# Optimization experiments

Hardware: AMD Instinct MI355X
Metric: run time of the kernel (lower is better)

Reference implementation:

```python
import jax, jax.numpy as jnp
from jax import lax
import numpy as np

D_COND = 48      # d_condition
K = 24           # n_bins
HID = 128        # hidden_dim
T = 10           # n_transforms
TAIL = 15.0      # tail_bound
B = 131072       # batch (contexts x samples flattened, as in sample())


def setup_inputs() -> dict:
    key = jax.random.key(0)
    ks = jax.random.split(key, 8)
    def w(k, shape, fan_in, gain=1.0):
        return (jax.random.normal(k, shape, jnp.float32) * (gain / np.sqrt(fan_in))).astype(jnp.float32)
    return {
        "z": jax.random.normal(ks[0], (B,), jnp.float32),
        "context": jax.random.normal(ks[1], (B, D_COND), jnp.float32),
        "W0": w(ks[2], (T, D_COND, HID), D_COND),
        "b0": jnp.zeros((T, HID), jnp.float32),
        "W1": w(ks[3], (T, HID, HID), HID),
        "b1": jnp.zeros((T, HID), jnp.float32),
        "W2": w(ks[4], (T, HID, HID), HID),
        "b2": jnp.zeros((T, HID), jnp.float32),
        "W3": w(ks[5], (T, HID, 3 * K + 1), HID, gain=0.1),
        "b3": jnp.zeros((T, 3 * K + 1), jnp.float32),
        "loc": jnp.float32(85.0),
        "scale": jnp.float32(5.0),
    }


def _spline_forward(x, widths, heights, derivs):
    # x: (B,); widths/heights: (B,K); derivs: (B,K+1)
    inside = (x >= -TAIL) & (x <= TAIL)
    cw = jnp.pad(jnp.cumsum(widths, -1), ((0, 0), (1, 0)), constant_values=-TAIL)   # (B,K+1)
    ch = jnp.pad(jnp.cumsum(heights, -1), ((0, 0), (1, 0)), constant_values=-TAIL)  # (B,K+1)
    # torch.searchsorted(cw[...,1:], x, right=False) == count of elems < x
    idx = jnp.clip(jnp.sum(cw[:, 1:] < x[:, None], axis=-1), 0, K - 1)
    take = lambda a, i: jnp.take_along_axis(a, i[:, None], axis=-1)[:, 0]
    w_k = take(widths, idx)
    h_k = take(heights, idx)
    cw_k = take(cw, idx)
    ch_k = take(ch, idx)
    d_k = take(derivs, idx)
    d_k1 = take(derivs, idx + 1)
    s = h_k / w_k
    xi = jnp.clip((x - cw_k) / w_k, 1e-6, 1.0 - 1e-6)
    one_m = 1.0 - xi
    numer = h_k * (s * xi * xi + d_k * xi * one_m)
    denom = s + (d_k + d_k1 - 2.0 * s) * xi * one_m
    y = ch_k + numer / denom
    dy_dxi = s * s * (d_k1 * xi * xi + 2.0 * s * xi * one_m + d_k * one_m * one_m) / (denom * denom)
    log_det = (jnp.log(jnp.maximum(dy_dxi, 1e-10))
               + jnp.log(jnp.maximum(h_k, 1e-10))
               - jnp.log(jnp.maximum(w_k, 1e-10)))
    y = jnp.where(inside, y, x)
    log_det = jnp.where(inside, log_det, 0.0)
    return y, log_det


def reference(z, context, W0, b0, W1, b1, W2, b2, W3, b3, loc, scale):
    def body(carry, p):
        zc, ld = carry
        w0, c0, w1, c1, w2, c2, w3, c3 = p
        h = jax.nn.silu(context @ w0 + c0)
        h = jax.nn.silu(h @ w1 + c1)
        h = jax.nn.silu(h @ w2 + c2)
        params = h @ w3 + c3                                   # (B, 3K+1)
        Wl, Hl, Dl = params[:, :K], params[:, K:2 * K], params[:, 2 * K:]
        widths = jax.nn.softmax(Wl, axis=-1) * (2.0 * TAIL)
        heights = jax.nn.softmax(Hl, axis=-1) * (2.0 * TAIL)
        derivs = jax.nn.softplus(Dl) + 1e-3
        y, l = _spline_forward(zc, widths, heights, derivs)
        return (y, ld + l), None

    (z_out, total_ld), _ = lax.scan(body, (z, jnp.zeros_like(z)),
                                    (W0, b0, W1, b1, W2, b2, W3, b3))
    s = jnp.maximum(scale, 0.1)
    temp_f = z_out * s + loc   # _unstandardize, as in sample()
    return temp_f, total_ld
```

## Files before the change

### kernel.cpp

```cpp
#include <hip/hip_runtime.h>
#include <hip/hip_bf16.h>

#define DCOND 48
#define KBINS 24
#define HID 128
#define TSTEPS 10
#define NPAR 73
#define TAILF 15.0f

typedef __attribute__((ext_vector_type(8))) short v8s;
typedef __attribute__((ext_vector_type(4))) float f32x4;
typedef __attribute__((ext_vector_type(4))) unsigned u32x4;

__device__ __forceinline__ short f2bf(float f) {
    __hip_bfloat16 h = __float2bfloat16(f);
    return __builtin_bit_cast(short, h);
}
__device__ __forceinline__ float bf2f(short s) {
    unsigned u = ((unsigned)(unsigned short)s) << 16;
    return __builtin_bit_cast(float, u);
}
__device__ __forceinline__ float silu_f(float v) {
    return __fdividef(v, 1.0f + __expf(-v));
}

__device__ __forceinline__ unsigned cvt_pk(float a, float b) {
    unsigned r;
    asm("v_cvt_pk_bf16_f32 %0, %1, %2" : "=v"(r) : "v"(a), "v"(b));
    return r;
}

__device__ __forceinline__ void split8(f32x4 a0, f32x4 a1, v8s& hi, v8s& lo) {
    unsigned h0 = cvt_pk(a0[0], a0[1]);
    unsigned h1 = cvt_pk(a0[2], a0[3]);
    unsigned h2 = cvt_pk(a1[0], a1[1]);
    unsigned h3 = cvt_pk(a1[2], a1[3]);
    float l0 = a0[0] - __builtin_bit_cast(float, h0 << 16);
    float l1 = a0[1] - __builtin_bit_cast(float, h0 & 0xffff0000u);
    float l2 = a0[2] - __builtin_bit_cast(float, h1 << 16);
    float l3 = a0[3] - __builtin_bit_cast(float, h1 & 0xffff0000u);
    float l4 = a1[0] - __builtin_bit_cast(float, h2 << 16);
    float l5 = a1[1] - __builtin_bit_cast(float, h2 & 0xffff0000u);
    float l6 = a1[2] - __builtin_bit_cast(float, h3 << 16);
    float l7 = a1[3] - __builtin_bit_cast(float, h3 & 0xffff0000u);
    unsigned q0 = cvt_pk(l0, l1);
    unsigned q1 = cvt_pk(l2, l3);
    unsigned q2 = cvt_pk(l4, l5);
    unsigned q3 = cvt_pk(l6, l7);
    hi = __builtin_bit_cast(v8s, (u32x4){h0, h1, h2, h3});
    lo = __builtin_bit_cast(v8s, (u32x4){q0, q1, q2, q3});
}

__global__ void prep_w(const float* __restrict__ W0, const float* __restrict__ W1,
                       const float* __restrict__ W2, const float* __restrict__ W3,
                       short* __restrict__ ws)
{
    int g = blockIdx.x * 256 + threadIdx.x;
    if (g >= TSTEPS * 51200) return;
    int t = g / 51200;
    int r = g % 51200;

    int base_e, elems, NT, Kreal, Nreal;
    const float* W;
    if (r < 8192)       { base_e = 0;     elems = 8192;  NT = 8; Kreal = 48;  Nreal = 128; W = W0 + (size_t)t * DCOND * HID; }
    else if (r < 24576) { base_e = 8192;  elems = 16384; NT = 8; Kreal = 128; Nreal = 128; W = W1 + (size_t)t * HID * HID; }
    else if (r < 40960) { base_e = 24576; elems = 16384; NT = 8; Kreal = 128; Nreal = 128; W = W2 + (size_t)t * HID * HID; }
    else                { base_e = 40960; elems = 10240; NT = 5; Kreal = 128; Nreal = 73;  W = W3 + (size_t)t * HID * NPAR; }

    int e  = r - base_e;
    int j  = e & 7;
    int ln = (e >> 3) & 63;
    int q  = e >> 9;
    int nt = q % NT, kc = q / NT;
    int k  = kc * 32 + (ln >> 4) * 8 + j;
    int n  = nt * 16 + (ln & 15);

    float v = 0.0f;
    if (k < Kreal && n < Nreal) v = W[(size_t)k * Nreal + n];
    short hi = f2bf(v);
    short lo = f2bf(v - bf2f(hi));

    size_t o = (size_t)t * 102400 + 2 * (size_t)base_e + e;
    ws[o]         = hi;
    ws[o + elems] = lo;
}

#define MBLK 128
#define NTHR 512

template<int ROUNDS>
__device__ __forceinline__ void w_issue(const short* __restrict__ g, int tid, v8s (&r)[8]) {
    #pragma unroll
    for (int i = 0; i < ROUNDS; ++i)
        r[i] = *(const v8s*)(g + tid * 8 + i * 4096);
}
template<int ROUNDS>
__device__ __forceinline__ void w_flush(short* __restrict__ lds, int tid, const v8s (&r)[8]) {
    #pragma unroll
    for (int i = 0; i < ROUNDS; ++i)
        *(v8s*)(lds + tid * 8 + i * 4096) = r[i];
}

template<int KC, int NTN, int NTOT, int ELEMS, bool ACT, bool AREG>
__device__ __forceinline__ void layer_run(const float* __restrict__ bias, int nreal,
                                          char* __restrict__ hb,
                                          const short* __restrict__ Wbh,
                                          int lane, int nb0,
                                          const v8s* cxh, const v8s* cxl)
{
    const int kg = (lane >> 4) * 8;

    v8s ah[2][KC], al[2][KC];
    #pragma unroll
    for (int mt = 0; mt < 2; ++mt) {
        const int arow = mt * 16 + (lane & 15);
        const int asw  = (arow & 7) << 4;
        #pragma unroll
        for (int kc = 0; kc < KC; ++kc) {
            if (AREG) {
                ah[mt][kc] = cxh[mt * KC + kc];
                al[mt][kc] = cxl[mt * KC + kc];
            } else {
                const int kb = (kc * 32 + kg) * 4;
                f32x4 a0 = *(const f32x4*)(hb + arow * 512 + (kb ^ asw));
                f32x4 a1 = *(const f32x4*)(hb + arow * 512 + ((kb + 16) ^ asw));
                split8(a0, a1, ah[mt][kc], al[mt][kc]);
            }
        }
    }

    const int ncol  = lane & 15;
    const int crow  = (lane >> 4) * 4;
    const short* bbase = Wbh + lane * 8;

    #pragma unroll
    for (int np = 0; np < NTN / 2; ++np) {
        const int n0 = nb0 + np * 32 + ncol;
        const int n1 = n0 + 16;
        const float bv0 = (n0 < nreal) ? bias[n0] : 0.0f;
        const float bv1 = (n1 < nreal) ? bias[n1] : 0.0f;
        f32x4 a00 = {bv0, bv0, bv0, bv0}, a01 = {bv1, bv1, bv1, bv1};
        f32x4 a10 = {bv0, bv0, bv0, bv0}, a11 = {bv1, bv1, bv1, bv1};
        #pragma unroll
        for (int kc = 0; kc < KC; ++kc) {
            const short* bp0 = bbase + (kc * NTOT + np * 2) * 512;
            const short* bp1 = bp0 + 512;
            v8s bh0 = *(const v8s*)bp0;
            v8s bl0 = *(const v8s*)(bp0 + ELEMS);
            v8s bh1 = *(const v8s*)bp1;
            v8s bl1 = *(const v8s*)(bp1 + ELEMS);
            a00 = __builtin_amdgcn_mfma_f32_16x16x32_bf16(ah[0][kc], bh0, a00, 0, 0, 0);
            a01 = __builtin_amdgcn_mfma_f32_16x16x32_bf16(ah[0][kc], bh1, a01, 0, 0, 0);
            a10 = __builtin_amdgcn_mfma_f32_16x16x32_bf16(ah[1][kc], bh0, a10, 0, 0, 0);
            a11 = __builtin_amdgcn_mfma_f32_16x16x32_bf16(ah[1][kc], bh1, a11, 0, 0, 0);
            a00 = __builtin_amdgcn_mfma_f32_16x16x32_bf16(ah[0][kc], bl0, a00, 0, 0, 0);
            a01 = __builtin_amdgcn_mfma_f32_16x16x32_bf16(ah[0][kc], bl1, a01, 0, 0, 0);
            a10 = __builtin_amdgcn_mfma_f32_16x16x32_bf16(ah[1][kc], bl0, a10, 0, 0, 0);
            a11 = __builtin_amdgcn_mfma_f32_16x16x32_bf16(ah[1][kc], bl1, a11, 0, 0, 0);
            a00 = __builtin_amdgcn_mfma_f32_16x16x32_bf16(al[0][kc], bh0, a00, 0, 0, 0);
            a01 = __builtin_amdgcn_mfma_f32_16x16x32_bf16(al[0][kc], bh1, a01, 0, 0, 0);
            a10 = __builtin_amdgcn_mfma_f32_16x16x32_bf16(al[1][kc], bh0, a10, 0, 0, 0);
            a11 = __builtin_amdgcn_mfma_f32_16x16x32_bf16(al[1][kc], bh1, a11, 0, 0, 0);
        }
        #pragma unroll
        for (int mt = 0; mt < 2; ++mt) {
            const f32x4 c0 = mt ? a10 : a00;
            const f32x4 c1 = mt ? a11 : a01;
            #pragma unroll
            for (int r = 0; r < 4; ++r) {
                const int row = mt * 16 + crow + r;
                const int sw  = (row & 7) << 4;
                float v0 = c0[r], v1 = c1[r];
                if (ACT) { v0 = silu_f(v0); v1 = silu_f(v1); }
                *(float*)(hb + row * 512 + ((n0 * 4) ^ sw)) = v0;
                *(float*)(hb + row * 512 + ((n1 * 4) ^ sw)) = v1;
            }
        }
    }
    if (NTN & 1) {
        const int n0 = nb0 + (NTN - 1) * 16 + ncol;
        const float bv0 = (n0 < nreal) ? bias[n0] : 0.0f;
        f32x4 a00 = {bv0, bv0, bv0, bv0};
        f32x4 a10 = {bv0, bv0, bv0, bv0};
        #pragma unroll
        for (int kc = 0; kc < KC; ++kc) {
            const short* bp0 = bbase + (kc * NTOT + NTN - 1) * 512;
            v8s bh0 = *(const v8s*)bp0;
            v8s bl0 = *(const v8s*)(bp0 + ELEMS);
            a00 = __builtin_amdgcn_mfma_f32_16x16x32_bf16(ah[0][kc], bh0, a00, 0, 0, 0);
            a10 = __builtin_amdgcn_mfma_f32_16x16x32_bf16(ah[1][kc], bh0, a10, 0, 0, 0);
            a00 = __builtin_amdgcn_mfma_f32_16x16x32_bf16(ah[0][kc], bl0, a00, 0, 0, 0);
            a10 = __builtin_amdgcn_mfma_f32_16x16x32_bf16(ah[1][kc], bl0, a10, 0, 0, 0);
            a00 = __builtin_amdgcn_mfma_f32_16x16x32_bf16(al[0][kc], bh0, a00, 0, 0, 0);
            a10 = __builtin_amdgcn_mfma_f32_16x16x32_bf16(al[1][kc], bh0, a10, 0, 0, 0);
        }
        #pragma unroll
        for (int mt = 0; mt < 2; ++mt) {
            const f32x4 c0 = mt ? a10 : a00;
            #pragma unroll
            for (int r = 0; r < 4; ++r) {
                const int row = mt * 16 + crow + r;
                const int sw  = (row & 7) << 4;
                float v0 = c0[r];
                if (ACT) v0 = silu_f(v0);
                *(float*)(hb + row * 512 + ((n0 * 4) ^ sw)) = v0;
            }
        }
    }
}

__global__ __launch_bounds__(NTHR, 2)
void nsf_mfma(const float* __restrict__ z_g, const float* __restrict__ ctx_g,
              const float* __restrict__ b0g, const float* __restrict__ b1g,
              const float* __restrict__ b2g, const float* __restrict__ b3g,
              const float* __restrict__ locp, const float* __restrict__ sclp,
              const short* __restrict__ wsW, float* __restrict__ out, int B)
{
    __shared__ float Hlds[MBLK * 128];
    __shared__ short Wlds[32768];
    const int tid  = threadIdx.x;
    const int lane = tid & 63, wave = tid >> 6;
    const int p    = wave >> 1, h = wave & 1;
    const int blk  = blockIdx.x;
    char* hb = (char*)Hlds + p * 32 * 512;

    v8s wreg[8];
    w_issue<4>(wsW, tid, wreg);

    v8s cxh[4], cxl[4];
    {
        const int k0 = (lane >> 4) * 8;
        #pragma unroll
        for (int mt = 0; mt < 2; ++mt) {
            int gidr = blk * MBLK + p * 32 + mt * 16 + (lane & 15);
            if (gidr > B - 1) gidr = B - 1;
            const float* cg = ctx_g + (size_t)gidr * DCOND;
            f32x4 c0 = *(const f32x4*)(cg + k0);
            f32x4 c1 = *(const f32x4*)(cg + k0 + 4);
            split8(c0, c1, cxh[mt * 2 + 0], cxl[mt * 2 + 0]);
            if ((lane >> 4) < 2) {
                f32x4 c2 = *(const f32x4*)(cg + 32 + k0);
                f32x4 c3 = *(const f32x4*)(cg + 36 + k0);
                split8(c2, c3, cxh[mt * 2 + 1], cxl[mt * 2 + 1]);
            } else {
                #pragma unroll
                for (int u = 0; u < 8; ++u) { cxh[mt * 2 + 1][u] = 0; cxl[mt * 2 + 1][u] = 0; }
            }
        }
    }

    float x = 0.0f, ld = 0.0f;
    if (lane < 16) {
        int gid = blk * MBLK + p * 32 + h * 16 + lane;
        if (gid > B - 1) gid = B - 1;
        x = z_g[gid];
    }

    #pragma unroll 1
    for (int t = 0; t < TSTEPS; ++t) {
        const short* wstep = wsW + (size_t)t * 102400;
        const short* wnext = wsW + (size_t)((t + 1) % TSTEPS) * 102400;

        w_flush<4>(Wlds, tid, wreg);
        w_issue<8>(wstep + 16384, tid, wreg);
        __syncthreads();

        layer_run<2, 4, 8, 8192, true, true>(b0g + t * HID, HID, hb,
                                             Wlds + h * 2048, lane, h * 64, cxh, cxl);
        __syncthreads();

        w_flush<8>(Wlds, tid, wreg);
        w_issue<8>(wstep + 49152, tid, wreg);
        __syncthreads();

        layer_run<4, 4, 8, 16384, true, false>(b1g + t * HID, HID, hb,
                                               Wlds + h * 2048, lane, h * 64, nullptr, nullptr);
        __syncthreads();

        w_flush<8>(Wlds, tid, wreg);
        w_issue<5>(wstep + 81920, tid, wreg);
        __syncthreads();

        layer_run<4, 4, 8, 16384, true, false>(b2g + t * HID, HID, hb,
                                               Wlds + h * 2048, lane, h * 64, nullptr, nullptr);
        __syncthreads();

        w_flush<5>(Wlds, tid, wreg);
        w_issue<4>(wnext, tid, wreg);
        __syncthreads();

        if (h == 0)
            layer_run<4, 3, 5, 10240, false, false>(b3g + t * NPAR, NPAR, hb,
                                                    Wlds, lane, 0, nullptr, nullptr);
        else
            layer_run<4, 2, 5, 10240, false, false>(b3g + t * NPAR, NPAR, hb,
                                                    Wlds + 1536, lane, 48, nullptr, nullptr);
        __syncthreads();

        if (lane < 16) {
            const int srow = h * 16 + lane;
            const char* hrow = hb + srow * 512;
            const int sw = (srow & 7) << 4;

            float pw[KBINS], ph[KBINS];
            #pragma unroll
            for (int g = 0; g < 6; ++g) {
                f32x4 vw = *(const f32x4*)(hrow + ((g * 16) ^ sw));
                f32x4 vh = *(const f32x4*)(hrow + (((g + 6) * 16) ^ sw));
                #pragma unroll
                for (int u = 0; u < 4; ++u) { pw[g * 4 + u] = vw[u]; ph[g * 4 + u] = vh[u]; }
            }
            float mw = pw[0], mh = ph[0];
            #pragma unroll
            for (int i = 1; i < KBINS; ++i) { mw = fmaxf(mw, pw[i]); mh = fmaxf(mh, ph[i]); }
            float wsum = 0.0f, hsum = 0.0f;
            #pragma unroll
            for (int i = 0; i < KBINS; ++i) {
                pw[i] = __expf(pw[i] - mw); wsum += pw[i];
                ph[i] = __expf(ph[i] - mh); hsum += ph[i];
            }
            const float wmul = __fdividef(2.0f * TAILF, wsum);
            const float hmul = __fdividef(2.0f * TAILF, hsum);

            float cw = 0.0f, ch = 0.0f;
            float cwk = -TAILF, chk = -TAILF;
            float wk = pw[0] * wmul, hk = ph[0] * hmul;
            int idx = 0;
            #pragma unroll
            for (int i = 1; i < KBINS; ++i) {
                cw += pw[i - 1] * wmul;
                ch += ph[i - 1] * hmul;
                if (cw < x) {
                    cwk = cw; chk = ch;
                    wk = pw[i] * wmul; hk = ph[i] * hmul;
                    idx = i;
                }
            }
            float d0 = *(const float*)(hrow + (((2 * KBINS + idx) * 4) ^ sw));
            float d1 = *(const float*)(hrow + (((2 * KBINS + idx + 1) * 4) ^ sw));
            const float dk  = fmaxf(d0, 0.0f) + __logf(1.0f + __expf(-fabsf(d0))) + 0.001f;
            const float dk1 = fmaxf(d1, 0.0f) + __logf(1.0f + __expf(-fabsf(d1))) + 0.001f;

            const bool inside = (x >= -TAILF) && (x <= TAILF);
            const float sr = __fdividef(hk, wk);
            float xi = __fdividef(x - cwk, wk);
            xi = fminf(fmaxf(xi, 1e-6f), 1.0f - 1e-6f);
            const float om  = 1.0f - xi;
            const float xio = xi * om;
            const float numer = hk * (sr * xi * xi + dk * xio);
            const float denom = sr + (dk + dk1 - 2.0f * sr) * xio;
            const float y = chk + __fdividef(numer, denom);
            const float dyd = __fdividef(sr * sr * (dk1 * xi * xi + 2.0f * sr * xio + dk * om * om),
                                         denom * denom);
            const float lg = __logf(fmaxf(dyd, 1e-10f)) + __logf(fmaxf(hk, 1e-10f))
                           - __logf(fmaxf(wk, 1e-10f));
            x  = inside ? y : x;
            ld += inside ? lg : 0.0f;
        }
    }

    if (lane < 16) {
        const int gid = blk * MBLK + p * 32 + h * 16 + lane;
        if (gid < B) {
            const float s = fmaxf(sclp[0], 0.1f);
            out[gid]     = fmaf(x, s, locp[0]);
            out[B + gid] = ld;
        }
    }
}

#define FBLK 256
template<int KIN, int WS, int NOUT, bool ACT>
__device__ __forceinline__ void dense_chunk(const float* __restrict__ W,
                                            const float* __restrict__ bias,
                                            int j0, const float (&hin)[KIN],
                                            float* __restrict__ sb, int tid)
{
    #pragma unroll 1
    for (int jj = 0; jj < NOUT; jj += 8) {
        const int j = j0 + jj;
        float a[8];
        #pragma unroll
        for (int u = 0; u < 8; ++u) a[u] = bias[j + u];
        #pragma unroll
        for (int k = 0; k < KIN; ++k) {
            const float* w = W + k * WS + j;
            const float hk = hin[k];
            #pragma unroll
            for (int u = 0; u < 8; ++u) a[u] = fmaf(hk, w[u], a[u]);
        }
        #pragma unroll
        for (int u = 0; u < 8; ++u) {
            float v = ACT ? silu_f(a[u]) : a[u];
            sb[(jj + u) * FBLK + tid] = v;
        }
    }
}

__global__ __launch_bounds__(FBLK, 2)
void nsf_fwd_slow(const float* __restrict__ z_g, const float* __restrict__ ctx_g,
                  const float* __restrict__ W0g, const float* __restrict__ b0g,
                  const float* __restrict__ W1g, const float* __restrict__ b1g,
                  const float* __restrict__ W2g, const float* __restrict__ b2g,
                  const float* __restrict__ W3g, const float* __restrict__ b3g,
                  const float* __restrict__ locp, const float* __restrict__ sclp,
                  float* __restrict__ out, int B)
{
    __shared__ float sbuf[64 * FBLK];
    const int tid = threadIdx.x;
    const int gid = blockIdx.x * FBLK + tid;
    if (gid >= B) return;
    float x = z_g[gid], ld = 0.0f;
    #pragma unroll 1
    for (int t = 0; t < TSTEPS; ++t) {
        asm volatile("" ::: "memory");
        const float* W0 = W0g + (size_t)t * DCOND * HID;
        const float* b0 = b0g + (size_t)t * HID;
        const float* W1 = W1g + (size_t)t * HID * HID;
        const float* b1 = b1g + (size_t)t * HID;
        const float* W2 = W2g + (size_t)t * HID * HID;
        const float* b2 = b2g + (size_t)t * HID;
        const float* W3 = W3g + (size_t)t * HID * NPAR;
        const float* b3 = b3g + (size_t)t * NPAR;
        float ctx[DCOND];
        #pragma unroll
        for (int k = 0; k < DCOND; ++k) ctx[k] = ctx_g[(size_t)gid * DCOND + k];
        float h[HID];
        dense_chunk<DCOND, HID, 64, true>(W0, b0, 0, ctx, sbuf, tid);
        #pragma unroll
        for (int j = 0; j < 64; ++j) h[j] = sbuf[j * FBLK + tid];
        dense_chunk<DCOND, HID, 64, true>(W0, b0, 64, ctx, sbuf, tid);
        #pragma unroll
        for (int j = 0; j < 64; ++j) h[64 + j] = sbuf[j * FBLK + tid];
        #pragma unroll 1
        for (int l = 0; l < 2; ++l) {
            const float* W  = (l == 0) ? W1 : W2;
            const float* bb = (l == 0) ? b1 : b2;
            float hlo[64];
            dense_chunk<HID, HID, 64, true>(W, bb, 0, h, sbuf, tid);
            #pragma unroll
            for (int j = 0; j < 64; ++j) hlo[j] = sbuf[j * FBLK + tid];
            dense_chunk<HID, HID, 64, true>(W, bb, 64, h, sbuf, tid);
            #pragma unroll
            for (int j = 0; j < 64; ++j) h[64 + j] = sbuf[j * FBLK + tid];
            #pragma unroll
            for (int j = 0; j < 64; ++j) h[j] = hlo[j];
        }
        float p[NPAR];
        dense_chunk<HID, NPAR, 64, false>(W3, b3, 0, h, sbuf, tid);
        #pragma unroll
        for (int j = 0; j < 64; ++j) p[j] = sbuf[j * FBLK + tid];
        dense_chunk<HID, NPAR, 8, false>(W3, b3, 64, h, sbuf, tid);
        #pragma unroll
        for (int j = 0; j < 8; ++j) p[64 + j] = sbuf[j * FBLK + tid];
        {
            float a = b3[72];
            #pragma unroll
            for (int k = 0; k < HID; ++k) a = fmaf(h[k], W3[k * NPAR + 72], a);
            p[72] = a;
        }
        float mw = p[0];
        #pragma unroll
        for (int i = 1; i < KBINS; ++i) mw = fmaxf(mw, p[i]);
        float we[KBINS]; float wsum = 0.0f;
        #pragma unroll
        for (int i = 0; i < KBINS; ++i) { we[i] = __expf(p[i] - mw); wsum += we[i]; }
        const float wmul = __fdividef(2.0f * TAILF, wsum);
        float mh = p[KBINS];
        #pragma unroll
        for (int i = 1; i < KBINS; ++i) mh = fmaxf(mh, p[KBINS + i]);
        float he[KBINS]; float hsum = 0.0f;
        #pragma unroll
        for (int i = 0; i < KBINS; ++i) { he[i] = __expf(p[KBINS + i] - mh); hsum += he[i]; }
        const float hmul = __fdividef(2.0f * TAILF, hsum);
        float dvv[KBINS + 1];
        #pragma unroll
        for (int i = 0; i <= KBINS; ++i) {
            float xd = p[2 * KBINS + i];
            dvv[i] = fmaxf(xd, 0.0f) + __logf(1.0f + __expf(-fabsf(xd))) + 0.001f;
        }
        float cw = 0.0f, ch = 0.0f, cwk = -TAILF, chk = -TAILF;
        float wk = we[0] * wmul, hk = he[0] * hmul, dk = dvv[0], dk1 = dvv[1];
        #pragma unroll
        for (int i = 1; i < KBINS; ++i) {
            cw += we[i - 1] * wmul;
            ch += he[i - 1] * hmul;
            if (cw < x) {
                cwk = cw; chk = ch;
                wk = we[i] * wmul; hk = he[i] * hmul;
                dk = dvv[i]; dk1 = dvv[i + 1];
            }
        }
        const bool inside = (x >= -TAILF) && (x <= TAILF);
        const float sr = __fdividef(hk, wk);
        float xi = __fdividef(x - cwk, wk);
        xi = fminf(fmaxf(xi, 1e-6f), 1.0f - 1e-6f);
        const float om  = 1.0f - xi;
        const float xio = xi * om;
        const float numer = hk * (sr * xi * xi + dk * xio);
        const float denom = sr + (dk + dk1 - 2.0f * sr) * xio;
        const float y = chk + __fdividef(numer, denom);
        const float dyd = __fdividef(sr * sr * (dk1 * xi * xi + 2.0f * sr * xio + dk * om * om),
                                     denom * denom);
        const float lg = __logf(fmaxf(dyd, 1e-10f)) + __logf(fmaxf(hk, 1e-10f))
                       - __logf(fmaxf(wk, 1e-10f));
        x  = inside ? y : x;
        ld += inside ? lg : 0.0f;
    }
    const float s = fmaxf(sclp[0], 0.1f);
    out[gid]     = fmaf(x, s, locp[0]);
    out[B + gid] = ld;
}

extern "C" void kernel_launch(void* const* d_in, const int* in_sizes, int n_in,
                              void* d_out, int out_size, void* d_ws, size_t ws_size,
                              hipStream_t stream) {
    const float* z    = (const float*)d_in[0];
    const float* ctx  = (const float*)d_in[1];
    const float* W0   = (const float*)d_in[2];
    const float* b0   = (const float*)d_in[3];
    const float* W1   = (const float*)d_in[4];
    const float* b1   = (const float*)d_in[5];
    const float* W2   = (const float*)d_in[6];
    const float* b2   = (const float*)d_in[7];
    const float* W3   = (const float*)d_in[8];
    const float* b3   = (const float*)d_in[9];
    const float* loc  = (const float*)d_in[10];
    const float* scl  = (const float*)d_in[11];
    float* out = (float*)d_out;
    const int B = in_sizes[0];

    const size_t ws_need = (size_t)TSTEPS * 102400 * sizeof(short);
    if (ws_size < ws_need) {
        const int nblk = (B + FBLK - 1) / FBLK;
        hipLaunchKernelGGL(nsf_fwd_slow, dim3(nblk), dim3(FBLK), 0, stream,
                           z, ctx, W0, b0, W1, b1, W2, b2, W3, b3, loc, scl, out, B);
        return;
    }

    short* ws = (short*)d_ws;
    const int prep_total = TSTEPS * 51200;
    hipLaunchKernelGGL(prep_w, dim3((prep_total + 255) / 256), dim3(256), 0, stream,
                       W0, W1, W2, W3, ws);

    const int nblk = (B + MBLK - 1) / MBLK;
    hipLaunchKernelGGL(nsf_mfma, dim3(nblk), dim3(NTHR), 0, stream,
                       z, ctx, b0, b1, b2, b3, loc, scl, ws, out, B);
}
```

Baseline: 761.1 us.

## Stage weight panels with direct global-to-LDS loads instead of register prefetch

Replaces the register-held weight prefetch (global load into VGPRs, then flush to LDS) with global_load_lds direct transfers issued after each layer's barrier. The A-operand split is hoisted out of the MFMA routine so it runs while the panel load is in flight. This removes the register staging and the LDS write instructions, which may lower VGPR pressure. The cost is that each weight panel load is now exposed on the critical path between layers instead of being prefetched a full layer ahead, plus an extra barrier per step.

Measured after the change: 651.8 us. -14.4%, faster.

```diff
diff --git a/kernel.cpp b/kernel.cpp
--- a/kernel.cpp
+++ b/kernel.cpp
@@ -88,47 +88,47 @@
 #define MBLK 128
 #define NTHR 512
 
-template<int ROUNDS>
-__device__ __forceinline__ void w_issue(const short* __restrict__ g, int tid, v8s (&r)[8]) {
+template<int NISSUE>
+__device__ __forceinline__ void stage_panel(const short* __restrict__ g,
+                                            short* lds, int tid)
+{
+    const int wuni = (tid >> 6) << 9;
+    const int lofs = tid * 8;
     #pragma unroll
-    for (int i = 0; i < ROUNDS; ++i)
-        r[i] = *(const v8s*)(g + tid * 8 + i * 4096);
-}
-template<int ROUNDS>
-__device__ __forceinline__ void w_flush(short* __restrict__ lds, int tid, const v8s (&r)[8]) {
-    #pragma unroll
-    for (int i = 0; i < ROUNDS; ++i)
-        *(v8s*)(lds + tid * 8 + i * 4096) = r[i];
-}
-
-template<int KC, int NTN, int NTOT, int ELEMS, bool ACT, bool AREG>
-__device__ __forceinline__ void layer_run(const float* __restrict__ bias, int nreal,
-                                          char* __restrict__ hb,
-                                          const short* __restrict__ Wbh,
-                                          int lane, int nb0,
-                                          const v8s* cxh, const v8s* cxl)
+    for (int i = 0; i < NISSUE; ++i) {
+        __builtin_amdgcn_global_load_lds(
+            (const __attribute__((address_space(1))) void*)(g + i * 4096 + lofs),
+            (__attribute__((address_space(3))) void*)(lds + i * 4096 + wuni),
+            16, 0, 0);
+    }
+}
+
+template<int KC>
+__device__ __forceinline__ void a_split(const char* __restrict__ hb, int lane,
+                                        v8s (&ah)[2][4], v8s (&al)[2][4])
 {
     const int kg = (lane >> 4) * 8;
-
-    v8s ah[2][KC], al[2][KC];
     #pragma unroll
     for (int mt = 0; mt < 2; ++mt) {
         const int arow = mt * 16 + (lane & 15);
         const int asw  = (arow & 7) << 4;
         #pragma unroll
         for (int kc = 0; kc < KC; ++kc) {
-            if (AREG) {
-                ah[mt][kc] = cxh[mt * KC + kc];
-                al[mt][kc] = cxl[mt * KC + kc];
-            } else {
-                const int kb = (kc * 32 + kg) * 4;
-                f32x4 a0 = *(const f32x4*)(hb + arow * 512 + (kb ^ asw));
-                f32x4 a1 = *(const f32x4*)(hb + arow * 512 + ((kb + 16) ^ asw));
-                split8(a0, a1, ah[mt][kc], al[mt][kc]);
-            }
-        }
-    }
-
+            const int kb = (kc * 32 + kg) * 4;
+            f32x4 a0 = *(const f32x4*)(hb + arow * 512 + (kb ^ asw));
+            f32x4 a1 = *(const f32x4*)(hb + arow * 512 + ((kb + 16) ^ asw));
+            split8(a0, a1, ah[mt][kc], al[mt][kc]);
+        }
+    }
+}
+
+template<int KC, int NTN, int NTOT, int ELEMS, bool ACT, int AKC>
+__device__ __forceinline__ void layer_mfma(const float* __restrict__ bias, int nreal,
+                                           char* __restrict__ hb,
+                                           const short* __restrict__ Wbh,
+                                           int lane, int nb0,
+                                           const v8s (&ah)[2][AKC], const v8s (&al)[2][AKC])
+{
     const int ncol  = lane & 15;
     const int crow  = (lane >> 4) * 4;
     const short* bbase = Wbh + lane * 8;
@@ -224,10 +224,9 @@
     const int blk  = blockIdx.x;
     char* hb = (char*)Hlds + p * 32 * 512;
 
-    v8s wreg[8];
-    w_issue<4>(wsW, tid, wreg);
-
-    v8s cxh[4], cxl[4];
+    stage_panel<4>(wsW, Wlds, tid);
+
+    v8s cxh[2][2], cxl[2][2];
     {
         const int k0 = (lane >> 4) * 8;
         #pragma unroll
@@ -237,14 +236,14 @@
             const float* cg = ctx_g + (size_t)gidr * DCOND;
             f32x4 c0 = *(const f32x4*)(cg + k0);
             f32x4 c1 = *(const f32x4*)(cg + k0 + 4);
-            split8(c0, c1, cxh[mt * 2 + 0], cxl[mt * 2 + 0]);
+            split8(c0, c1, cxh[mt][0], cxl[mt][0]);
             if ((lane >> 4) < 2) {
                 f32x4 c2 = *(const f32x4*)(cg + 32 + k0);
                 f32x4 c3 = *(const f32x4*)(cg + 36 + k0);
-                split8(c2, c3, cxh[mt * 2 + 1], cxl[mt * 2 + 1]);
+                split8(c2, c3, cxh[mt][1], cxl[mt][1]);
             } else {
                 #pragma unroll
-                for (int u = 0; u < 8; ++u) { cxh[mt * 2 + 1][u] = 0; cxl[mt * 2 + 1][u] = 0; }
+                for (int u = 0; u < 8; ++u) { cxh[mt][1][u] = 0; cxl[mt][1][u] = 0; }
             }
         }
     }
@@ -256,46 +255,48 @@
         x = z_g[gid];
     }
 
+    v8s axh[2][4], axl[2][4];
+
+    __syncthreads();
+
     #pragma unroll 1
     for (int t = 0; t < TSTEPS; ++t) {
         const short* wstep = wsW + (size_t)t * 102400;
         const short* wnext = wsW + (size_t)((t + 1) % TSTEPS) * 102400;
 
-        w_flush<4>(Wlds, tid, wreg);
-        w_issue<8>(wstep + 16384, tid, wreg);
-        __syncthreads();
-
-        layer_run<2, 4, 8, 8192, true, true>(b0g + t * HID, HID, hb,
-                                             Wlds + h * 2048, lane, h * 64, cxh, cxl);
-        __syncthreads();
-
-        w_flush<8>(Wlds, tid, wreg);
-        w_issue<8>(wstep + 49152, tid, wreg);
-        __syncthreads();
-
-        layer_run<4, 4, 8, 16384, true, false>(b1g + t * HID, HID, hb,
-                                               Wlds + h * 2048, lane, h * 64, nullptr, nullptr);
-        __syncthreads();
-
-        w_flush<8>(Wlds, tid, wreg);
-        w_issue<5>(wstep + 81920, tid, wreg);
-        __syncthreads();
-
-        layer_run<4, 4, 8, 16384, true, false>(b2g + t * HID, HID, hb,
-                                               Wlds + h * 2048, lane, h * 64, nullptr, nullptr);
-        __syncthreads();
-
-        w_flush<5>(Wlds, tid, wreg);
-        w_issue<4>(wnext, tid, wreg);
+        layer_mfma<2, 4, 8, 8192, true, 2>(b0g + t * HID, HID, hb,
+                                           Wlds + h * 2048, lane, h * 64, cxh, cxl);
+        __syncthreads();
+
+        stage_panel<8>(wstep + 16384, Wlds, tid);
+        a_split<4>(hb, lane, axh, axl);
+        __syncthreads();
+
+        layer_mfma<4, 4, 8, 16384, true, 4>(b1g + t * HID, HID, hb,
+                                            Wlds + h * 2048, lane, h * 64, axh, axl);
+        __syncthreads();
+
+        stage_panel<8>(wstep + 49152, Wlds, tid);
+        a_split<4>(hb, lane, axh, axl);
+        __syncthreads();
+
+        layer_mfma<4, 4, 8, 16384, true, 4>(b2g + t * HID, HID, hb,
+                                            Wlds + h * 2048, lane, h * 64, axh, axl);
+        __syncthreads();
+
+        stage_panel<5>(wstep + 81920, Wlds, tid);
+        a_split<4>(hb, lane, axh, axl);
         __syncthreads();
 
         if (h == 0)
-            layer_run<4, 3, 5, 10240, false, false>(b3g + t * NPAR, NPAR, hb,
-                                                    Wlds, lane, 0, nullptr, nullptr);
+            layer_mfma<4, 3, 5, 10240, false, 4>(b3g + t * NPAR, NPAR, hb,
+                                                 Wlds, lane, 0, axh, axl);
         else
-            layer_run<4, 2, 5, 10240, false, false>(b3g + t * NPAR, NPAR, hb,
-                                                    Wlds + 1536, lane, 48, nullptr, nullptr);
-        __syncthreads();
+            layer_mfma<4, 2, 5, 10240, false, 4>(b3g + t * NPAR, NPAR, hb,
+                                                 Wlds + 1536, lane, 48, axh, axl);
+        __syncthreads();
+
+        stage_panel<4>(wnext, Wlds, tid);
 
         if (lane < 16) {
             const int srow = h * 16 + lane;
@@ -357,6 +358,7 @@
             x  = inside ? y : x;
             ld += inside ? lg : 0.0f;
         }
+        __syncthreads();
     }
 
     if (lane < 16) {
```
